# Optimization experiments

Measured on AMD Instinct MI355X. Metric: run time of the kernel, lower is better.

## Reference

```python
import jax, jax.numpy as jnp
import numpy as np
from jax import lax

HIDDEN = 1024; HEADS = 16; HEAD = 64; LAYERS = 4; MLP = 4096
PATCH = 16; TUBE = 2; CROP = 224; FRAMES = 16
GRID = CROP // PATCH          # 14
DEPTH = FRAMES // TUBE        # 8
N_TOK = DEPTH * GRID * GRID   # 1568
EPS = 1e-6
D_ROT = 2 * ((HEAD // 3) // 2)  # 20 per rotary axis (d, h, w); 4 dims left unrotated


def setup_inputs() -> dict:
    key = jax.random.key(0)
    ks = jax.random.split(key, 12)
    w = lambda k, shape: jax.random.normal(k, shape, jnp.float32) * 0.02
    L, H, M = LAYERS, HIDDEN, MLP
    return {
        "pixel_values_videos": jax.random.normal(ks[0], (2, FRAMES, 3, CROP, CROP), jnp.float32),
        "patch_w": w(ks[1], (H, 3, TUBE, PATCH, PATCH)),  # Conv3d OIDHW
        "patch_b": jnp.zeros((H,), jnp.float32),
        "ln1_g": jnp.ones((L, H), jnp.float32), "ln1_b": jnp.zeros((L, H), jnp.float32),
        "qw": w(ks[2], (L, H, H)), "qb": jnp.zeros((L, H), jnp.float32),
        "kw": w(ks[3], (L, H, H)), "kb": jnp.zeros((L, H), jnp.float32),
        "vw": w(ks[4], (L, H, H)), "vb": jnp.zeros((L, H), jnp.float32),
        "pw": w(ks[5], (L, H, H)), "pb": jnp.zeros((L, H), jnp.float32),
        "ln2_g": jnp.ones((L, H), jnp.float32), "ln2_b": jnp.zeros((L, H), jnp.float32),
        "fc1w": w(ks[6], (L, M, H)), "fc1b": jnp.zeros((L, M), jnp.float32),
        "fc2w": w(ks[7], (L, H, M)), "fc2b": jnp.zeros((L, H), jnp.float32),
        "lnf_g": jnp.ones((H,), jnp.float32), "lnf_b": jnp.zeros((H,), jnp.float32),
    }


def _layer_norm(x, g, b):
    mu = jnp.mean(x, axis=-1, keepdims=True)
    var = jnp.mean(jnp.square(x - mu), axis=-1, keepdims=True)
    return (x - mu) * lax.rsqrt(var + EPS) * g + b


def _position_ids():
    ids = jnp.arange(N_TOK)
    tpf = GRID * GRID
    d_pos = ids // tpf
    rem = ids - d_pos * tpf
    h_pos = rem // GRID
    w_pos = rem - h_pos * GRID
    return d_pos, h_pos, w_pos


def _rotate(x, pos):
    # x: (B, H, N, D); matches VJEPA2 rotate_queries_or_keys:
    # tiled (not interleaved) sin/cos * interleaved rotate-half.
    D = x.shape[-1]
    omega = 1.0 / (10000.0 ** (jnp.arange(D // 2, dtype=x.dtype) / (D / 2.0)))
    freq = pos.astype(x.dtype)[:, None] * omega              # (N, D/2)
    sin = jnp.concatenate([jnp.sin(freq)] * 2, axis=-1)      # (N, D) tiled (torch .repeat)
    cos = jnp.concatenate([jnp.cos(freq)] * 2, axis=-1)
    y = x.reshape(x.shape[:-1] + (D // 2, 2))
    y = jnp.stack([-y[..., 1], y[..., 0]], axis=-1).reshape(x.shape)
    return x * cos + y * sin


def _apply_rope(x, pos_ids):
    d_pos, h_pos, w_pos = pos_ids
    s0, s1, s2 = 0, D_ROT, 2 * D_ROT
    parts = [_rotate(x[..., s0:s1], d_pos), _rotate(x[..., s1:s2], h_pos),
             _rotate(x[..., s2:3 * D_ROT], w_pos)]
    if 3 * D_ROT < HEAD:
        parts.append(x[..., 3 * D_ROT:])
    return jnp.concatenate(parts, axis=-1)


def _forward(pixel_values_videos, patch_w, patch_b, ln1_g, ln1_b, qw, qb, kw, kb,
             vw, vb, pw, pb, ln2_g, ln2_b, fc1w, fc1b, fc2w, fc2b, lnf_g, lnf_b):
    B = pixel_values_videos.shape[0]
    x = jnp.transpose(pixel_values_videos, (0, 2, 1, 3, 4))  # (B, C, T, H, W)
    h = lax.conv_general_dilated(x, patch_w, window_strides=(TUBE, PATCH, PATCH),
                                 padding="VALID",
                                 dimension_numbers=("NCDHW", "OIDHW", "NCDHW"))
    h = h + patch_b[None, :, None, None, None]
    h = h.reshape(B, HIDDEN, -1).transpose(0, 2, 1)          # (B, N, HIDDEN)

    pos_ids = _position_ids()
    scale = HEAD ** -0.5

    for i in range(LAYERS):
        # attention block
        xn = _layer_norm(h, ln1_g[i], ln1_b[i])
        def heads(w_, b_):
            return (xn @ w_.T + b_).reshape(B, N_TOK, HEADS, HEAD).transpose(0, 2, 1, 3)
        q = _apply_rope(heads(qw[i], qb[i]), pos_ids)
        k = _apply_rope(heads(kw[i], kb[i]), pos_ids)
        v = heads(vw[i], vb[i])
        aw = jnp.einsum("bhnd,bhmd->bhnm", q, k) * scale
        aw = jax.nn.softmax(aw.astype(jnp.float32), axis=-1).astype(q.dtype)
        o = jnp.einsum("bhnm,bhmd->bhnd", aw, v)
        o = o.transpose(0, 2, 1, 3).reshape(B, N_TOK, HIDDEN)
        h = h + (o @ pw[i].T + pb[i])
        # MLP block
        xn = _layer_norm(h, ln2_g[i], ln2_b[i])
        m = jax.nn.gelu(xn @ fc1w[i].T + fc1b[i], approximate=False)
        h = h + (m @ fc2w[i].T + fc2b[i])

    return _layer_norm(h, lnf_g, lnf_b)


def reference(pixel_values_videos, patch_w, patch_b, ln1_g, ln1_b, qw, qb, kw, kb,
              vw, vb, pw, pb, ln2_g, ln2_b, fc1w, fc1b, fc2w, fc2b, lnf_g, lnf_b):
    return _forward(pixel_values_videos, patch_w, patch_b, ln1_g, ln1_b, qw, qb, kw, kb,
                    vw, vb, pw, pb, ln2_g, ln2_b, fc1w, fc1b, fc2w, fc2b, lnf_g, lnf_b)
```

## Files before the change

### kernel.cpp

```cpp
#include <hip/hip_runtime.h>
#include <math.h>

#define NTOK   1568
#define BATCH  2
#define HID    1024
#define MLPD   4096
#define NLAYER 4
#define ROWS   (BATCH*NTOK)
#define CONVK  1536

typedef __bf16 bf16x8 __attribute__((ext_vector_type(8)));
typedef float  f32x4  __attribute__((ext_vector_type(4)));

__device__ __forceinline__ unsigned short f2b(float f) {
  unsigned int u = __float_as_uint(f);
  unsigned int r = u + 0x7FFFu + ((u >> 16) & 1u);
  return (unsigned short)(r >> 16);
}
__device__ __forceinline__ float b2f(unsigned short s) {
  return __uint_as_float((unsigned int)s << 16);
}

__device__ __forceinline__ void async16(const unsigned short* g, unsigned short* l) {
  __builtin_amdgcn_global_load_lds(
      (__attribute__((address_space(1))) void*)(void*)g,
      (__attribute__((address_space(3))) void*)(void*)l, 16, 0, 0);
}

__global__ __launch_bounds__(256) void cast4_k(const float* __restrict__ s,
                                               unsigned short* __restrict__ d,
                                               long long n4) {
  long long i = (long long)blockIdx.x * 256 + threadIdx.x;
  long long stride = (long long)gridDim.x * 256;
  for (; i < n4; i += stride) {
    float4 v = ((const float4*)s)[i];
    *(ushort4*)(d + i * 4) = make_ushort4(f2b(v.x), f2b(v.y), f2b(v.z), f2b(v.w));
  }
}

__global__ __launch_bounds__(256) void castqkv_k(const float* __restrict__ q,
                                                 const float* __restrict__ k,
                                                 const float* __restrict__ v,
                                                 unsigned short* __restrict__ dst) {
  const float* src = blockIdx.y == 0 ? q : (blockIdx.y == 1 ? k : v);
  long long i4 = (long long)blockIdx.x * 256 + threadIdx.x;
  long long e = i4 * 4;
  int layer = (int)(e >> 20);
  long long de = e + ((long long)(2 * layer + blockIdx.y) << 20);
  float4 val = ((const float4*)src)[i4];
  *(ushort4*)(dst + de) = make_ushort4(f2b(val.x), f2b(val.y), f2b(val.z), f2b(val.w));
}

__global__ __launch_bounds__(256) void biascat_k(const float* __restrict__ qb,
                                                 const float* __restrict__ kb,
                                                 const float* __restrict__ vb,
                                                 float* __restrict__ dst) {
  int idx = blockIdx.x * 256 + threadIdx.x;
  int layer = idx / 3072, c = idx % 3072;
  float v = c < 1024 ? qb[layer * 1024 + c]
            : (c < 2048 ? kb[layer * 1024 + c - 1024] : vb[layer * 1024 + c - 2048]);
  dst[idx] = v;
}

__global__ __launch_bounds__(256) void im2col_k(const float* __restrict__ pv,
                                                unsigned short* __restrict__ A) {
  int idx = blockIdx.x * 256 + threadIdx.x;
  int row = idx / CONVK, col = idx % CONVK;
  int b = row / NTOK, t = row % NTOK;
  int d = t / 196, r = t % 196, hh = r / 14, ww = r % 14;
  int c = col >> 9, r2 = col & 511, td = r2 >> 8, ph = (r2 >> 4) & 15, pw = r2 & 15;
  int frame = 2 * d + td;
  const float* src = pv + ((((long long)b * 16 + frame) * 3 + c) * 224 + (hh * 16 + ph)) * 224
                        + (ww * 16 + pw);
  A[idx] = f2b(*src);
}

__global__ __launch_bounds__(256) void gemm_bt(const unsigned short* __restrict__ A,
                                               const unsigned short* __restrict__ B,
                                               unsigned short* __restrict__ outP,
                                               int M, int N, int K, int kChunk) {
  __shared__ unsigned short As[2][128 * 32];
  __shared__ unsigned short Bs[2][128 * 32];
  const int tid = threadIdx.x;
  const int lane = tid & 63;
  const int w = tid >> 6;
  const int wm = (w >> 1) * 64, wn = (w & 1) * 64;
  const int l15 = lane & 15, l4 = lane >> 4;
  const int bm = blockIdx.y, bn = blockIdx.x;
  const int wbase = tid & ~63;
  const int kbeg = blockIdx.z * kChunk;

  auto stage = [&](int buf, int k0) {
#pragma unroll
    for (int it = 0; it < 2; ++it) {
      int c = it * 256 + tid;
      int rowA = bm * 128 + (c >> 2);
      if (rowA >= M) rowA = M - 1;
      async16(A + (size_t)rowA * K + k0 + (c & 3) * 8, &As[buf][(it * 256 + wbase) * 8]);
      int rowB = bn * 128 + (c >> 2);
      async16(B + (size_t)rowB * K + k0 + (c & 3) * 8, &Bs[buf][(it * 256 + wbase) * 8]);
    }
  };

  f32x4 acc[4][4] = {};
  stage(0, kbeg);
  const int nIter = kChunk >> 5;

  for (int i = 0; i < nIter; ++i) {
    const int cur = i & 1;
    __syncthreads();
    if (i + 1 < nIter) stage(cur ^ 1, kbeg + (i + 1) * 32);

    bf16x8 af[4], bfr[4];
#pragma unroll
    for (int ii = 0; ii < 4; ++ii)
      af[ii] = *(const bf16x8*)&As[cur][(wm + ii * 16 + l15) * 32 + l4 * 8];
#pragma unroll
    for (int j = 0; j < 4; ++j)
      bfr[j] = *(const bf16x8*)&Bs[cur][(wn + j * 16 + l15) * 32 + l4 * 8];
#pragma unroll
    for (int ii = 0; ii < 4; ++ii)
#pragma unroll
      for (int j = 0; j < 4; ++j)
        acc[ii][j] = __builtin_amdgcn_mfma_f32_16x16x32_bf16(af[ii], bfr[j], acc[ii][j], 0, 0, 0);
  }

  unsigned short* pout = outP + (size_t)blockIdx.z * ((size_t)M * N);
#pragma unroll
  for (int ii = 0; ii < 4; ++ii) {
    int rowb = bm * 128 + wm + ii * 16 + l4 * 4;
#pragma unroll
    for (int r = 0; r < 4; ++r) {
      int rr = rowb + r;
      if (rr >= M) continue;
#pragma unroll
      for (int j = 0; j < 4; ++j) {
        int col = bn * 128 + wn + j * 16 + l15;
        pout[(size_t)rr * N + col] = f2b(acc[ii][j][r]);
      }
    }
  }
}

template <int NP, int RESID, int GELU, int OUTB>
__global__ __launch_bounds__(256) void reduceN_k(const unsigned short* __restrict__ p,
                                                 const float* __restrict__ bias,
                                                 const float* __restrict__ resid,
                                                 float* __restrict__ outF,
                                                 unsigned short* __restrict__ outB,
                                                 int MN, int N) {
  int i8 = blockIdx.x * 256 + threadIdx.x;
  int e = i8 * 8;
  float acc[8];
#pragma unroll
  for (int j = 0; j < 8; ++j) acc[j] = 0.0f;
#pragma unroll
  for (int pp = 0; pp < NP; ++pp) {
    const unsigned short* src = p + (size_t)pp * MN + e;
    ushort4 a0 = *(const ushort4*)src;
    ushort4 a1 = *(const ushort4*)(src + 4);
    acc[0] += b2f(a0.x); acc[1] += b2f(a0.y); acc[2] += b2f(a0.z); acc[3] += b2f(a0.w);
    acc[4] += b2f(a1.x); acc[5] += b2f(a1.y); acc[6] += b2f(a1.z); acc[7] += b2f(a1.w);
  }
  int col = e % N;
  float4 b0 = *(const float4*)(bias + col);
  float4 b1 = *(const float4*)(bias + col + 4);
  acc[0] += b0.x; acc[1] += b0.y; acc[2] += b0.z; acc[3] += b0.w;
  acc[4] += b1.x; acc[5] += b1.y; acc[6] += b1.z; acc[7] += b1.w;
  if (RESID) {
    float4 r0 = *(const float4*)(resid + e);
    float4 r1 = *(const float4*)(resid + e + 4);
    acc[0] += r0.x; acc[1] += r0.y; acc[2] += r0.z; acc[3] += r0.w;
    acc[4] += r1.x; acc[5] += r1.y; acc[6] += r1.z; acc[7] += r1.w;
  }
  if (GELU) {
#pragma unroll
    for (int j = 0; j < 8; ++j)
      acc[j] = 0.5f * acc[j] * (1.0f + erff(acc[j] * 0.70710678118654752f));
  }
  if (OUTB) {
    *(ushort4*)(outB + e) = make_ushort4(f2b(acc[0]), f2b(acc[1]), f2b(acc[2]), f2b(acc[3]));
    *(ushort4*)(outB + e + 4) = make_ushort4(f2b(acc[4]), f2b(acc[5]), f2b(acc[6]), f2b(acc[7]));
  } else {
    *(float4*)(outF + e) = make_float4(acc[0], acc[1], acc[2], acc[3]);
    *(float4*)(outF + e + 4) = make_float4(acc[4], acc[5], acc[6], acc[7]);
  }
}

template <int OUT_BF16>
__global__ __launch_bounds__(256) void ln_k(const float* __restrict__ x,
                                            const float* __restrict__ g,
                                            const float* __restrict__ b,
                                            unsigned short* __restrict__ oB,
                                            float* __restrict__ oF) {
  __shared__ float red[8];
  const int row = blockIdx.x, tid = threadIdx.x;
  const float4 v = ((const float4*)(x + (size_t)row * HID))[tid];
  float s = v.x + v.y + v.z + v.w;
  float q = v.x * v.x + v.y * v.y + v.z * v.z + v.w * v.w;
  for (int off = 32; off; off >>= 1) { s += __shfl_xor(s, off); q += __shfl_xor(q, off); }
  if ((tid & 63) == 0) { red[tid >> 6] = s; red[4 + (tid >> 6)] = q; }
  __syncthreads();
  float ts = red[0] + red[1] + red[2] + red[3];
  float tq = red[4] + red[5] + red[6] + red[7];
  float mu = ts * (1.0f / HID);
  float var = tq * (1.0f / HID) - mu * mu;
  float rs = rsqrtf(var + 1e-6f);
  int col = tid * 4;
  float o0 = (v.x - mu) * rs * g[col + 0] + b[col + 0];
  float o1 = (v.y - mu) * rs * g[col + 1] + b[col + 1];
  float o2 = (v.z - mu) * rs * g[col + 2] + b[col + 2];
  float o3 = (v.w - mu) * rs * g[col + 3] + b[col + 3];
  if (OUT_BF16) {
    *(ushort4*)(oB + (size_t)row * HID + col) = make_ushort4(f2b(o0), f2b(o1), f2b(o2), f2b(o3));
  } else {
    *(float4*)(oF + (size_t)row * HID + col) = make_float4(o0, o1, o2, o3);
  }
}

__global__ __launch_bounds__(256) void qkvprep_k(const unsigned short* __restrict__ qkvb,
                                                 unsigned short* __restrict__ Qh,
                                                 unsigned short* __restrict__ Kh,
                                                 unsigned short* __restrict__ VT) {
  __shared__ unsigned short Vs[64 * 72];
  const int tile = blockIdx.x, bh = blockIdx.y;
  const int b = bh >> 4, head = bh & 15;
  const int tid = threadIdx.x;
  const int tl = tid >> 2, dc = tid & 3;
  const int tg = tile * 64 + tl;
  const int trc = tg < NTOK ? tg : NTOK - 1;
  const bool valid = tg < NTOK;
  const size_t srow = ((size_t)(b * NTOK + trc)) * 3072 + head * 64 + dc * 16;

  {
    uint4 v0 = *(const uint4*)(qkvb + srow + 2048);
    uint4 v1 = *(const uint4*)(qkvb + srow + 2048 + 8);
    *(uint4*)&Vs[tl * 72 + dc * 16] = v0;
    *(uint4*)&Vs[tl * 72 + dc * 16 + 8] = v1;
  }

  const int t = trc;
  const int dpos = t / 196, rem = t - dpos * 196, hpos = rem / 14, wpos = rem - hpos * 14;
  const float LG = 0.9210340371976184f;
  union V16 { uint4 u[2]; unsigned short s[16]; };
  V16 qin, kin, qout, kout;
  qin.u[0] = *(const uint4*)(qkvb + srow);
  qin.u[1] = *(const uint4*)(qkvb + srow + 8);
  kin.u[0] = *(const uint4*)(qkvb + srow + 1024);
  kin.u[1] = *(const uint4*)(qkvb + srow + 1024 + 8);
#pragma unroll
  for (int p = 0; p < 8; ++p) {
    int d0 = dc * 16 + 2 * p;
    float qx0 = b2f(qin.s[2 * p]), qx1 = b2f(qin.s[2 * p + 1]);
    float kx0 = b2f(kin.s[2 * p]), kx1 = b2f(kin.s[2 * p + 1]);
    float qo0, qo1, ko0, ko1;
    if (d0 >= 60) { qo0 = qx0; qo1 = qx1; ko0 = kx0; ko1 = kx1; }
    else {
      int region = d0 / 20;
      int j0 = d0 - region * 20;
      int pos = region == 0 ? dpos : (region == 1 ? hpos : wpos);
      float fp = (float)pos;
      int i0 = j0 % 10, i1 = (j0 + 1) % 10;
      float f0 = expf(-LG * (float)i0) * fp;
      float f1 = expf(-LG * (float)i1) * fp;
      float c0 = cosf(f0), s0 = sinf(f0), c1 = cosf(f1), s1 = sinf(f1);
      qo0 = qx0 * c0 - qx1 * s0; qo1 = qx1 * c1 + qx0 * s1;
      ko0 = kx0 * c0 - kx1 * s0; ko1 = kx1 * c1 + kx0 * s1;
    }
    qout.s[2 * p]     = f2b(qo0 * 0.125f);
    qout.s[2 * p + 1] = f2b(qo1 * 0.125f);
    kout.s[2 * p]     = f2b(ko0);
    kout.s[2 * p + 1] = f2b(ko1);
  }
  if (valid) {
    size_t drow = ((size_t)bh * NTOK + tg) * 64 + dc * 16;
    *(uint4*)(Qh + drow)     = qout.u[0];
    *(uint4*)(Qh + drow + 8) = qout.u[1];
    *(uint4*)(Kh + drow)     = kout.u[0];
    *(uint4*)(Kh + drow + 8) = kout.u[1];
  }
  __syncthreads();
  {
    int d = tid >> 2, tc = tid & 3;
    if (tile * 64 + tc * 16 < NTOK) {
      V16 o;
#pragma unroll
      for (int jj = 0; jj < 16; ++jj) o.s[jj] = Vs[(tc * 16 + jj) * 72 + d];
      unsigned short* dst = VT + ((size_t)bh * 64 + d) * NTOK + tile * 64 + tc * 16;
      *(uint4*)dst = o.u[0];
      *(uint4*)(dst + 8) = o.u[1];
    }
  }
}

__global__ __launch_bounds__(256, 3) void flash4_k(const unsigned short* __restrict__ Qh,
                                                   const unsigned short* __restrict__ Kh,
                                                   const unsigned short* __restrict__ VT,
                                                   unsigned short* __restrict__ O) {
  __shared__ unsigned short Ks[2][64 * 64];
  __shared__ unsigned short Vs[2][64 * 64];
  __shared__ unsigned short Os[4][16 * 72];
  const int bh = blockIdx.x, qt = blockIdx.y;
  const int b = bh >> 4, head = bh & 15;
  const int tid = threadIdx.x, lane = tid & 63, w = tid >> 6;
  const int l15 = lane & 15, l4 = lane >> 4;
  const size_t hb = (size_t)bh * NTOK * 64;
  const unsigned short* kgp = Kh + hb;
  const unsigned short* vbp = VT + (size_t)bh * 64 * NTOK;

  const int srow0 = w * 8 + (lane >> 3);
  const int scg0  = (lane & 7) ^ (srow0 & 7);
  const int srow1 = srow0 + 32;
  const int scg1  = (lane & 7) ^ (srow1 & 7);

  const int qrow = qt * 64 + w * 16 + l15;
  const int qrc = qrow < NTOK ? qrow : NTOK - 1;
  bf16x8 q0 = *(const bf16x8*)(Qh + hb + (size_t)qrc * 64 + l4 * 8);
  bf16x8 q1 = *(const bf16x8*)(Qh + hb + (size_t)qrc * 64 + 32 + l4 * 8);

  f32x4 oacc[4] = {};
  float m = -1e30f, l = 0.0f;

  {
    async16(kgp + (size_t)srow0 * 64 + scg0 * 8, &Ks[0][(size_t)w * 512]);
    async16(kgp + (size_t)srow1 * 64 + scg1 * 8, &Ks[0][(size_t)(w + 4) * 512]);
    async16(vbp + (size_t)srow0 * NTOK + scg0 * 8, &Vs[0][(size_t)w * 512]);
    async16(vbp + (size_t)srow1 * NTOK + scg1 * 8, &Vs[0][(size_t)(w + 4) * 512]);
  }

  const int h7 = l15 & 7;
  const int p1 = (l4 ^ h7) * 8;
  const int p2 = ((l4 + 4) ^ h7) * 8;

  for (int kt = 0; kt < 25; ++kt) {
    const int cur = kt & 1, nxt = cur ^ 1;
    const int kb = kt * 64;
    __syncthreads();

    if (kt < 24) {
      const int kn = kb + 64;
      async16(kgp + (size_t)(kn + srow0) * 64 + scg0 * 8, &Ks[nxt][(size_t)w * 512]);
      async16(kgp + (size_t)(kn + srow1) * 64 + scg1 * 8, &Ks[nxt][(size_t)(w + 4) * 512]);
      async16(vbp + (size_t)srow0 * NTOK + kn + scg0 * 8, &Vs[nxt][(size_t)w * 512]);
      async16(vbp + (size_t)srow1 * NTOK + kn + scg1 * 8, &Vs[nxt][(size_t)(w + 4) * 512]);
    }

    bf16x8 kc0[4], kc1[4];
#pragma unroll
    for (int nt = 0; nt < 4; ++nt) {
      const unsigned short* kr = &Ks[cur][(nt * 16 + l15) * 64];
      kc0[nt] = *(const bf16x8*)(kr + p1);
      kc1[nt] = *(const bf16x8*)(kr + p2);
    }
    f32x4 s[4] = {};
#pragma unroll
    for (int nt = 0; nt < 4; ++nt) {
      s[nt] = __builtin_amdgcn_mfma_f32_16x16x32_bf16(kc0[nt], q0, s[nt], 0, 0, 0);
      s[nt] = __builtin_amdgcn_mfma_f32_16x16x32_bf16(kc1[nt], q1, s[nt], 0, 0, 0);
    }
    bf16x8 vf0[4], vf1[4];
#pragma unroll
    for (int dt = 0; dt < 4; ++dt) {
      const unsigned short* vr = &Vs[cur][(dt * 16 + l15) * 64];
      vf0[dt] = *(const bf16x8*)(vr + p1);
      vf1[dt] = *(const bf16x8*)(vr + p2);
    }

    if (kb + 64 > NTOK) {
#pragma unroll
      for (int nt = 0; nt < 4; ++nt)
#pragma unroll
        for (int r = 0; r < 4; ++r)
          if (kb + nt * 16 + l4 * 4 + r >= NTOK) s[nt][r] = -1e30f;
    }
    float rmax = s[0][0];
#pragma unroll
    for (int nt = 0; nt < 4; ++nt)
#pragma unroll
      for (int r = 0; r < 4; ++r) rmax = fmaxf(rmax, s[nt][r]);
    rmax = fmaxf(rmax, __shfl_xor(rmax, 16));
    rmax = fmaxf(rmax, __shfl_xor(rmax, 32));
    float mn = fmaxf(m, rmax);
    float alpha = __expf(m - mn);
    m = mn;
    float rsum = 0.0f;
#pragma unroll
    for (int nt = 0; nt < 4; ++nt)
#pragma unroll
      for (int r = 0; r < 4; ++r) {
        float p = __expf(s[nt][r] - mn);
        s[nt][r] = p;
        rsum += p;
      }
    rsum += __shfl_xor(rsum, 16);
    rsum += __shfl_xor(rsum, 32);
    l = l * alpha + rsum;
#pragma unroll
    for (int dt = 0; dt < 4; ++dt)
#pragma unroll
      for (int r = 0; r < 4; ++r) oacc[dt][r] *= alpha;

    unsigned pk01[4], pk23[4];
#pragma unroll
    for (int nt = 0; nt < 4; ++nt) {
      pk01[nt] = (unsigned)f2b(s[nt][0]) | ((unsigned)f2b(s[nt][1]) << 16);
      pk23[nt] = (unsigned)f2b(s[nt][2]) | ((unsigned)f2b(s[nt][3]) << 16);
    }
    const int srcA = ((l4 & 1) << 5) | l15;
    const int srcB = srcA + 16;
    const bool hi = (l4 >> 1) != 0;
    union PB { unsigned u[4]; bf16x8 v; } pf[2];
#pragma unroll
    for (int kc = 0; kc < 2; ++kc) {
      unsigned t0, t1;
      t0 = __shfl(pk01[2 * kc], srcA); t1 = __shfl(pk01[2 * kc + 1], srcA);
      pf[kc].u[0] = hi ? t1 : t0;
      t0 = __shfl(pk23[2 * kc], srcA); t1 = __shfl(pk23[2 * kc + 1], srcA);
      pf[kc].u[1] = hi ? t1 : t0;
      t0 = __shfl(pk01[2 * kc], srcB); t1 = __shfl(pk01[2 * kc + 1], srcB);
      pf[kc].u[2] = hi ? t1 : t0;
      t0 = __shfl(pk23[2 * kc], srcB); t1 = __shfl(pk23[2 * kc + 1], srcB);
      pf[kc].u[3] = hi ? t1 : t0;
    }
#pragma unroll
    for (int dt = 0; dt < 4; ++dt) {
      oacc[dt] = __builtin_amdgcn_mfma_f32_16x16x32_bf16(vf0[dt], pf[0].v, oacc[dt], 0, 0, 0);
      oacc[dt] = __builtin_amdgcn_mfma_f32_16x16x32_bf16(vf1[dt], pf[1].v, oacc[dt], 0, 0, 0);
    }
  }

  float inv = 1.0f / l;
#pragma unroll
  for (int dt = 0; dt < 4; ++dt)
#pragma unroll
    for (int r = 0; r < 4; ++r)
      Os[w][l15 * 72 + dt * 16 + l4 * 4 + r] = f2b(oacc[dt][r] * inv);
  if (qrow < NTOK) {
    uint4 a  = *(const uint4*)&Os[w][l15 * 72 + l4 * 16];
    uint4 bq = *(const uint4*)&Os[w][l15 * 72 + l4 * 16 + 8];
    unsigned short* op = O + ((size_t)(b * NTOK + qrow)) * HID + head * 64;
    *(uint4*)(op + l4 * 16) = a;
    *(uint4*)(op + l4 * 16 + 8) = bq;
  }
}

extern "C" void kernel_launch(void* const* d_in, const int* in_sizes, int n_in,
                              void* d_out, int out_size, void* d_ws, size_t ws_size,
                              hipStream_t stream) {
  (void)in_sizes; (void)n_in; (void)out_size; (void)ws_size;
  const float* pv      = (const float*)d_in[0];
  const float* patch_w = (const float*)d_in[1];
  const float* patch_b = (const float*)d_in[2];
  const float* ln1_g   = (const float*)d_in[3];
  const float* ln1_b   = (const float*)d_in[4];
  const float* qw = (const float*)d_in[5];
  const float* qb = (const float*)d_in[6];
  const float* kw = (const float*)d_in[7];
  const float* kb = (const float*)d_in[8];
  const float* vw = (const float*)d_in[9];
  const float* vb = (const float*)d_in[10];
  const float* pw = (const float*)d_in[11];
  const float* pb = (const float*)d_in[12];
  const float* ln2_g = (const float*)d_in[13];
  const float* ln2_b = (const float*)d_in[14];
  const float* fc1w = (const float*)d_in[15];
  const float* fc1b = (const float*)d_in[16];
  const float* fc2w = (const float*)d_in[17];
  const float* fc2b = (const float*)d_in[18];
  const float* lnf_g = (const float*)d_in[19];
  const float* lnf_b = (const float*)d_in[20];

  char* wsp = (char*)d_ws;
  auto alloc = [&](size_t bytes) {
    char* p = wsp;
    wsp += (bytes + 255) & ~(size_t)255;
    return p;
  };
  unsigned short* wPatch = (unsigned short*)alloc((size_t)1024 * 1536 * 2);
  unsigned short* wQKV   = (unsigned short*)alloc((size_t)NLAYER * 3072 * 1024 * 2);
  unsigned short* wP     = (unsigned short*)alloc((size_t)NLAYER * HID * HID * 2);
  unsigned short* wF1    = (unsigned short*)alloc((size_t)NLAYER * MLPD * HID * 2);
  unsigned short* wF2    = (unsigned short*)alloc((size_t)NLAYER * HID * MLPD * 2);
  float*          qkvbias = (float*)alloc((size_t)NLAYER * 3072 * 4);
  unsigned short* Aim  = (unsigned short*)alloc((size_t)ROWS * CONVK * 2);
  float*          h    = (float*)alloc((size_t)ROWS * HID * 4);
  unsigned short* xnb  = (unsigned short*)alloc((size_t)ROWS * HID * 2);
  unsigned short* qkvo = (unsigned short*)alloc((size_t)ROWS * 3072 * 2);
  unsigned short* Qh   = (unsigned short*)alloc((size_t)ROWS * HID * 2 + 8192);
  unsigned short* Kh   = (unsigned short*)alloc((size_t)ROWS * HID * 2 + 8192);
  unsigned short* VT   = (unsigned short*)alloc((size_t)ROWS * HID * 2 + 8192);
  unsigned short* ob   = (unsigned short*)alloc((size_t)ROWS * HID * 2);
  unsigned short* mb   = (unsigned short*)alloc((size_t)ROWS * MLPD * 2);
  unsigned short* part = Qh;

  const int MN = ROWS * HID;

  auto cast = [&](const float* s, unsigned short* d, long long n) {
    long long n4 = n / 4;
    int grid = (int)((n4 + 255) / 256);
    if (grid > 16384) grid = 16384;
    cast4_k<<<grid, 256, 0, stream>>>(s, d, n4);
  };
  cast(patch_w, wPatch, (long long)1024 * 1536);
  castqkv_k<<<dim3(4096, 3), 256, 0, stream>>>(qw, kw, vw, wQKV);
  cast(pw, wP, (long long)NLAYER * HID * HID);
  cast(fc1w, wF1, (long long)NLAYER * MLPD * HID);
  cast(fc2w, wF2, (long long)NLAYER * HID * MLPD);
  biascat_k<<<48, 256, 0, stream>>>(qb, kb, vb, qkvbias);

  im2col_k<<<(ROWS * CONVK) / 256, 256, 0, stream>>>(pv, Aim);
  gemm_bt<<<dim3(8, 25, 3), 256, 0, stream>>>(Aim, wPatch, part, ROWS, HID, CONVK, 512);
  reduceN_k<3, 0, 0, 0><<<MN / 2048, 256, 0, stream>>>(
      part, patch_b, nullptr, h, nullptr, MN, HID);

  for (int i = 0; i < NLAYER; ++i) {
    ln_k<1><<<ROWS, 256, 0, stream>>>(h, ln1_g + i * HID, ln1_b + i * HID, xnb, nullptr);
    gemm_bt<<<dim3(24, 25, 2), 256, 0, stream>>>(
        xnb, wQKV + (size_t)i * 3072 * 1024, part, ROWS, 3072, HID, 512);
    reduceN_k<2, 0, 0, 1><<<(ROWS * 3072) / 2048, 256, 0, stream>>>(
        part, qkvbias + i * 3072, nullptr, nullptr, qkvo, ROWS * 3072, 3072);
    qkvprep_k<<<dim3(25, 32), 256, 0, stream>>>(qkvo, Qh, Kh, VT);
    flash4_k<<<dim3(32, 25), 256, 0, stream>>>(Qh, Kh, VT, ob);
    gemm_bt<<<dim3(8, 25, 4), 256, 0, stream>>>(
        ob, wP + (size_t)i * HID * HID, part, ROWS, HID, HID, 256);
    reduceN_k<4, 1, 0, 0><<<MN / 2048, 256, 0, stream>>>(
        part, pb + i * HID, h, h, nullptr, MN, HID);
    ln_k<1><<<ROWS, 256, 0, stream>>>(h, ln2_g + i * HID, ln2_b + i * HID, xnb, nullptr);
    gemm_bt<<<dim3(32, 25, 2), 256, 0, stream>>>(
        xnb, wF1 + (size_t)i * MLPD * HID, part, ROWS, MLPD, HID, 512);
    reduceN_k<2, 0, 1, 1><<<(ROWS * MLPD) / 2048, 256, 0, stream>>>(
        part, fc1b + i * MLPD, nullptr, nullptr, mb, ROWS * MLPD, MLPD);
    gemm_bt<<<dim3(8, 25, 4), 256, 0, stream>>>(
        mb, wF2 + (size_t)i * HID * MLPD, part, ROWS, HID, MLPD, 1024);
    reduceN_k<4, 1, 0, 0><<<MN / 2048, 256, 0, stream>>>(
        part, fc2b + i * HID, h, h, nullptr, MN, HID);
  }
  ln_k<0><<<ROWS, 256, 0, stream>>>(h, lnf_g, lnf_b, nullptr, (float*)d_out);
}
```

Before: 1.505 ms.

## Fuse split-K reduction with LayerNorm and split attention KV across two blocks

Replaces the separate split-K reduce plus LayerNorm kernels with one redln_k that sums partials, adds bias and residual, writes h and emits the normalized bf16 activations, including the final LayerNorm. This removes a full read/write pass over the hidden state per residual point. Attention is split into two KV halves (flash5_k, grid z=2, higher occupancy bound) with a combine kernel that merges the partial outputs using the saved max and sum, adding parallelism at the cost of an extra bf16 partial round-trip. Partial buffers are re-aliased across existing allocations with explicit strides, which depends on careful buffer lifetime reasoning.

```diff
diff --git a/kernel.cpp b/kernel.cpp
--- a/kernel.cpp
+++ b/kernel.cpp
@@ -77,8 +77,9 @@
 
 __global__ __launch_bounds__(256) void gemm_bt(const unsigned short* __restrict__ A,
                                                const unsigned short* __restrict__ B,
-                                               unsigned short* __restrict__ outP,
-                                               int M, int N, int K, int kChunk) {
+                                               unsigned short* outP,
+                                               int M, int N, int K, int kChunk,
+                                               size_t zStride) {
   __shared__ unsigned short As[2][128 * 32];
   __shared__ unsigned short Bs[2][128 * 32];
   const int tid = threadIdx.x;
@@ -125,7 +126,7 @@
         acc[ii][j] = __builtin_amdgcn_mfma_f32_16x16x32_bf16(af[ii], bfr[j], acc[ii][j], 0, 0, 0);
   }
 
-  unsigned short* pout = outP + (size_t)blockIdx.z * ((size_t)M * N);
+  unsigned short* pout = outP + (size_t)blockIdx.z * zStride;
 #pragma unroll
   for (int ii = 0; ii < 4; ++ii) {
     int rowb = bm * 128 + wm + ii * 16 + l4 * 4;
@@ -142,13 +143,11 @@
   }
 }
 
-template <int NP, int RESID, int GELU, int OUTB>
-__global__ __launch_bounds__(256) void reduceN_k(const unsigned short* __restrict__ p,
+template <int NP, int GELU>
+__global__ __launch_bounds__(256) void reduceN_k(const unsigned short* p,
                                                  const float* __restrict__ bias,
-                                                 const float* __restrict__ resid,
-                                                 float* __restrict__ outF,
-                                                 unsigned short* __restrict__ outB,
-                                                 int MN, int N) {
+                                                 unsigned short* outB,
+                                                 int MN, int N, size_t pStride) {
   int i8 = blockIdx.x * 256 + threadIdx.x;
   int e = i8 * 8;
   float acc[8];
@@ -156,7 +155,7 @@
   for (int j = 0; j < 8; ++j) acc[j] = 0.0f;
 #pragma unroll
   for (int pp = 0; pp < NP; ++pp) {
-    const unsigned short* src = p + (size_t)pp * MN + e;
+    const unsigned short* src = p + (size_t)pp * pStride + e;
     ushort4 a0 = *(const ushort4*)src;
     ushort4 a1 = *(const ushort4*)(src + 4);
     acc[0] += b2f(a0.x); acc[1] += b2f(a0.y); acc[2] += b2f(a0.z); acc[3] += b2f(a0.w);
@@ -167,38 +166,45 @@
   float4 b1 = *(const float4*)(bias + col + 4);
   acc[0] += b0.x; acc[1] += b0.y; acc[2] += b0.z; acc[3] += b0.w;
   acc[4] += b1.x; acc[5] += b1.y; acc[6] += b1.z; acc[7] += b1.w;
-  if (RESID) {
-    float4 r0 = *(const float4*)(resid + e);
-    float4 r1 = *(const float4*)(resid + e + 4);
-    acc[0] += r0.x; acc[1] += r0.y; acc[2] += r0.z; acc[3] += r0.w;
-    acc[4] += r1.x; acc[5] += r1.y; acc[6] += r1.z; acc[7] += r1.w;
-  }
   if (GELU) {
 #pragma unroll
     for (int j = 0; j < 8; ++j)
       acc[j] = 0.5f * acc[j] * (1.0f + erff(acc[j] * 0.70710678118654752f));
   }
-  if (OUTB) {
-    *(ushort4*)(outB + e) = make_ushort4(f2b(acc[0]), f2b(acc[1]), f2b(acc[2]), f2b(acc[3]));
-    *(ushort4*)(outB + e + 4) = make_ushort4(f2b(acc[4]), f2b(acc[5]), f2b(acc[6]), f2b(acc[7]));
-  } else {
-    *(float4*)(outF + e) = make_float4(acc[0], acc[1], acc[2], acc[3]);
-    *(float4*)(outF + e + 4) = make_float4(acc[4], acc[5], acc[6], acc[7]);
-  }
-}
-
-template <int OUT_BF16>
-__global__ __launch_bounds__(256) void ln_k(const float* __restrict__ x,
-                                            const float* __restrict__ g,
-                                            const float* __restrict__ b,
-                                            unsigned short* __restrict__ oB,
-                                            float* __restrict__ oF) {
+  *(ushort4*)(outB + e) = make_ushort4(f2b(acc[0]), f2b(acc[1]), f2b(acc[2]), f2b(acc[3]));
+  *(ushort4*)(outB + e + 4) = make_ushort4(f2b(acc[4]), f2b(acc[5]), f2b(acc[6]), f2b(acc[7]));
+}
+
+template <int NP, int RESID, int FINAL>
+__global__ __launch_bounds__(256) void redln_k(const unsigned short* __restrict__ p,
+                                               const float* __restrict__ bias,
+                                               const float* resid,
+                                               const float* __restrict__ g,
+                                               const float* __restrict__ b,
+                                               float* hOut,
+                                               unsigned short* __restrict__ xnOut,
+                                               float* __restrict__ fOut,
+                                               size_t pStride) {
   __shared__ float red[8];
   const int row = blockIdx.x, tid = threadIdx.x;
-  const float4 v = ((const float4*)(x + (size_t)row * HID))[tid];
-  float s = v.x + v.y + v.z + v.w;
-  float q = v.x * v.x + v.y * v.y + v.z * v.z + v.w * v.w;
-  for (int off = 32; off; off >>= 1) { s += __shfl_xor(s, off); q += __shfl_xor(q, off); }
+  const int col = tid * 4;
+  const size_t off = (size_t)row * HID + col;
+  float v0 = 0, v1 = 0, v2 = 0, v3 = 0;
+#pragma unroll
+  for (int pp = 0; pp < NP; ++pp) {
+    ushort4 a = *(const ushort4*)(p + (size_t)pp * pStride + off);
+    v0 += b2f(a.x); v1 += b2f(a.y); v2 += b2f(a.z); v3 += b2f(a.w);
+  }
+  float4 bs = *(const float4*)(bias + col);
+  v0 += bs.x; v1 += bs.y; v2 += bs.z; v3 += bs.w;
+  if (RESID) {
+    float4 r = *(const float4*)(resid + off);
+    v0 += r.x; v1 += r.y; v2 += r.z; v3 += r.w;
+  }
+  if (!FINAL) *(float4*)(hOut + off) = make_float4(v0, v1, v2, v3);
+  float s = v0 + v1 + v2 + v3;
+  float q = v0 * v0 + v1 * v1 + v2 * v2 + v3 * v3;
+  for (int o2 = 32; o2; o2 >>= 1) { s += __shfl_xor(s, o2); q += __shfl_xor(q, o2); }
   if ((tid & 63) == 0) { red[tid >> 6] = s; red[4 + (tid >> 6)] = q; }
   __syncthreads();
   float ts = red[0] + red[1] + red[2] + red[3];
@@ -206,15 +212,14 @@
   float mu = ts * (1.0f / HID);
   float var = tq * (1.0f / HID) - mu * mu;
   float rs = rsqrtf(var + 1e-6f);
-  int col = tid * 4;
-  float o0 = (v.x - mu) * rs * g[col + 0] + b[col + 0];
-  float o1 = (v.y - mu) * rs * g[col + 1] + b[col + 1];
-  float o2 = (v.z - mu) * rs * g[col + 2] + b[col + 2];
-  float o3 = (v.w - mu) * rs * g[col + 3] + b[col + 3];
-  if (OUT_BF16) {
-    *(ushort4*)(oB + (size_t)row * HID + col) = make_ushort4(f2b(o0), f2b(o1), f2b(o2), f2b(o3));
+  float o0 = (v0 - mu) * rs * g[col + 0] + b[col + 0];
+  float o1 = (v1 - mu) * rs * g[col + 1] + b[col + 1];
+  float o2 = (v2 - mu) * rs * g[col + 2] + b[col + 2];
+  float o3 = (v3 - mu) * rs * g[col + 3] + b[col + 3];
+  if (FINAL) {
+    *(float4*)(fOut + off) = make_float4(o0, o1, o2, o3);
   } else {
-    *(float4*)(oF + (size_t)row * HID + col) = make_float4(o0, o1, o2, o3);
+    *(ushort4*)(xnOut + off) = make_ushort4(f2b(o0), f2b(o1), f2b(o2), f2b(o3));
   }
 }
 
@@ -293,15 +298,15 @@
   }
 }
 
-__global__ __launch_bounds__(256, 3) void flash4_k(const unsigned short* __restrict__ Qh,
+__global__ __launch_bounds__(256, 4) void flash5_k(const unsigned short* __restrict__ Qh,
                                                    const unsigned short* __restrict__ Kh,
                                                    const unsigned short* __restrict__ VT,
-                                                   unsigned short* __restrict__ O) {
+                                                   unsigned short* __restrict__ Opart,
+                                                   float2* __restrict__ ml) {
   __shared__ unsigned short Ks[2][64 * 64];
   __shared__ unsigned short Vs[2][64 * 64];
-  __shared__ unsigned short Os[4][16 * 72];
-  const int bh = blockIdx.x, qt = blockIdx.y;
-  const int b = bh >> 4, head = bh & 15;
+  const int bh = blockIdx.x, qt = blockIdx.y, kv = blockIdx.z;
+  const int kt0 = kv ? 13 : 0, kt1 = kv ? 25 : 13;
   const int tid = threadIdx.x, lane = tid & 63, w = tid >> 6;
   const int l15 = lane & 15, l4 = lane >> 4;
   const size_t hb = (size_t)bh * NTOK * 64;
@@ -322,22 +327,23 @@
   float m = -1e30f, l = 0.0f;
 
   {
-    async16(kgp + (size_t)srow0 * 64 + scg0 * 8, &Ks[0][(size_t)w * 512]);
-    async16(kgp + (size_t)srow1 * 64 + scg1 * 8, &Ks[0][(size_t)(w + 4) * 512]);
-    async16(vbp + (size_t)srow0 * NTOK + scg0 * 8, &Vs[0][(size_t)w * 512]);
-    async16(vbp + (size_t)srow1 * NTOK + scg1 * 8, &Vs[0][(size_t)(w + 4) * 512]);
+    const int kc0 = kt0 * 64;
+    async16(kgp + (size_t)(kc0 + srow0) * 64 + scg0 * 8, &Ks[0][(size_t)w * 512]);
+    async16(kgp + (size_t)(kc0 + srow1) * 64 + scg1 * 8, &Ks[0][(size_t)(w + 4) * 512]);
+    async16(vbp + (size_t)srow0 * NTOK + kc0 + scg0 * 8, &Vs[0][(size_t)w * 512]);
+    async16(vbp + (size_t)srow1 * NTOK + kc0 + scg1 * 8, &Vs[0][(size_t)(w + 4) * 512]);
   }
 
   const int h7 = l15 & 7;
   const int p1 = (l4 ^ h7) * 8;
   const int p2 = ((l4 + 4) ^ h7) * 8;
 
-  for (int kt = 0; kt < 25; ++kt) {
-    const int cur = kt & 1, nxt = cur ^ 1;
+  for (int kt = kt0; kt < kt1; ++kt) {
+    const int cur = (kt - kt0) & 1, nxt = cur ^ 1;
     const int kb = kt * 64;
     __syncthreads();
 
-    if (kt < 24) {
+    if (kt + 1 < kt1) {
       const int kn = kb + 64;
       async16(kgp + (size_t)(kn + srow0) * 64 + scg0 * 8, &Ks[nxt][(size_t)w * 512]);
       async16(kgp + (size_t)(kn + srow1) * 64 + scg1 * 8, &Ks[nxt][(size_t)(w + 4) * 512]);
@@ -429,19 +435,48 @@
     }
   }
 
-  float inv = 1.0f / l;
+  __syncthreads();
+  unsigned short* Os = &Ks[0][0];
 #pragma unroll
   for (int dt = 0; dt < 4; ++dt)
 #pragma unroll
     for (int r = 0; r < 4; ++r)
-      Os[w][l15 * 72 + dt * 16 + l4 * 4 + r] = f2b(oacc[dt][r] * inv);
+      Os[w * 1152 + l15 * 72 + dt * 16 + l4 * 4 + r] = f2b(oacc[dt][r]);
   if (qrow < NTOK) {
-    uint4 a  = *(const uint4*)&Os[w][l15 * 72 + l4 * 16];
-    uint4 bq = *(const uint4*)&Os[w][l15 * 72 + l4 * 16 + 8];
-    unsigned short* op = O + ((size_t)(b * NTOK + qrow)) * HID + head * 64;
+    uint4 a  = *(const uint4*)&Os[w * 1152 + l15 * 72 + l4 * 16];
+    uint4 bq = *(const uint4*)&Os[w * 1152 + l15 * 72 + l4 * 16 + 8];
+    unsigned short* op = Opart + ((size_t)(kv * 32 + bh) * NTOK + qrow) * 64;
     *(uint4*)(op + l4 * 16) = a;
     *(uint4*)(op + l4 * 16 + 8) = bq;
-  }
+    if (l4 == 0) ml[(size_t)(kv * 32 + bh) * NTOK + qrow] = make_float2(m, l);
+  }
+}
+
+__global__ __launch_bounds__(256) void fcomb_k(const unsigned short* __restrict__ Op,
+                                               const float2* __restrict__ ml,
+                                               unsigned short* __restrict__ O) {
+  const int bh = blockIdx.x, qt = blockIdx.y;
+  const int tid = threadIdx.x;
+  const int qr = qt * 64 + (tid >> 2);
+  const int dc = (tid & 3) * 16;
+  if (qr >= NTOK) return;
+  const int b = bh >> 4, head = bh & 15;
+  float2 a0 = ml[(size_t)bh * NTOK + qr];
+  float2 a1 = ml[(size_t)(32 + bh) * NTOK + qr];
+  float M = fmaxf(a0.x, a1.x);
+  float w0 = __expf(a0.x - M), w1 = __expf(a1.x - M);
+  float inv = 1.0f / (a0.y * w0 + a1.y * w1);
+  w0 *= inv; w1 *= inv;
+  union V16 { uint4 u[2]; unsigned short s[16]; } p0, p1, o;
+  const unsigned short* q0 = Op + ((size_t)bh * NTOK + qr) * 64 + dc;
+  const unsigned short* q1 = Op + ((size_t)(32 + bh) * NTOK + qr) * 64 + dc;
+  p0.u[0] = *(const uint4*)q0;       p0.u[1] = *(const uint4*)(q0 + 8);
+  p1.u[0] = *(const uint4*)q1;       p1.u[1] = *(const uint4*)(q1 + 8);
+#pragma unroll
+  for (int j = 0; j < 16; ++j) o.s[j] = f2b(b2f(p0.s[j]) * w0 + b2f(p1.s[j]) * w1);
+  unsigned short* dst = O + ((size_t)(b * NTOK + qr)) * HID + head * 64 + dc;
+  *(uint4*)dst = o.u[0];
+  *(uint4*)(dst + 8) = o.u[1];
 }
 
 extern "C" void kernel_launch(void* const* d_in, const int* in_sizes, int n_in,
@@ -491,9 +526,13 @@
   unsigned short* VT   = (unsigned short*)alloc((size_t)ROWS * HID * 2 + 8192);
   unsigned short* ob   = (unsigned short*)alloc((size_t)ROWS * HID * 2);
   unsigned short* mb   = (unsigned short*)alloc((size_t)ROWS * MLPD * 2);
-  unsigned short* part = Qh;
-
-  const int MN = ROWS * HID;
+
+  unsigned short* part  = Qh;
+  unsigned short* partM = mb;
+  unsigned short* Opart = mb;
+  float2*         mlbuf = (float2*)(mb + (size_t)2 * 32 * NTOK * 64);
+  const size_t MNs = (size_t)ROWS * HID;
+  const size_t strideF1 = (size_t)(mb - part);
 
   auto cast = [&](const float* s, unsigned short* d, long long n) {
     long long n4 = n / 4;
@@ -509,31 +548,36 @@
   biascat_k<<<48, 256, 0, stream>>>(qb, kb, vb, qkvbias);
 
   im2col_k<<<(ROWS * CONVK) / 256, 256, 0, stream>>>(pv, Aim);
-  gemm_bt<<<dim3(8, 25, 3), 256, 0, stream>>>(Aim, wPatch, part, ROWS, HID, CONVK, 512);
-  reduceN_k<3, 0, 0, 0><<<MN / 2048, 256, 0, stream>>>(
-      part, patch_b, nullptr, h, nullptr, MN, HID);
+  gemm_bt<<<dim3(8, 25, 3), 256, 0, stream>>>(Aim, wPatch, part, ROWS, HID, CONVK, 512, MNs);
+  redln_k<3, 0, 0><<<ROWS, 256, 0, stream>>>(
+      part, patch_b, nullptr, ln1_g, ln1_b, h, xnb, nullptr, MNs);
 
   for (int i = 0; i < NLAYER; ++i) {
-    ln_k<1><<<ROWS, 256, 0, stream>>>(h, ln1_g + i * HID, ln1_b + i * HID, xnb, nullptr);
     gemm_bt<<<dim3(24, 25, 2), 256, 0, stream>>>(
-        xnb, wQKV + (size_t)i * 3072 * 1024, part, ROWS, 3072, HID, 512);
-    reduceN_k<2, 0, 0, 1><<<(ROWS * 3072) / 2048, 256, 0, stream>>>(
-        part, qkvbias + i * 3072, nullptr, nullptr, qkvo, ROWS * 3072, 3072);
+        xnb, wQKV + (size_t)i * 3072 * 1024, part, ROWS, 3072, HID, 512,
+        (size_t)ROWS * 3072);
+    reduceN_k<2, 0><<<(ROWS * 3072) / 2048, 256, 0, stream>>>(
+        part, qkvbias + i * 3072, qkvo, ROWS * 3072, 3072, (size_t)ROWS * 3072);
     qkvprep_k<<<dim3(25, 32), 256, 0, stream>>>(qkvo, Qh, Kh, VT);
-    flash4_k<<<dim3(32, 25), 256, 0, stream>>>(Qh, Kh, VT, ob);
+    flash5_k<<<dim3(32, 25, 2), 256, 0, stream>>>(Qh, Kh, VT, Opart, mlbuf);
+    fcomb_k<<<dim3(32, 25), 256, 0, stream>>>(Opart, mlbuf, ob);
     gemm_bt<<<dim3(8, 25, 4), 256, 0, stream>>>(
-        ob, wP + (size_t)i * HID * HID, part, ROWS, HID, HID, 256);
-    reduceN_k<4, 1, 0, 0><<<MN / 2048, 256, 0, stream>>>(
-        part, pb + i * HID, h, h, nullptr, MN, HID);
-    ln_k<1><<<ROWS, 256, 0, stream>>>(h, ln2_g + i * HID, ln2_b + i * HID, xnb, nullptr);
+        ob, wP + (size_t)i * HID * HID, partM, ROWS, HID, HID, 256, MNs);
+    redln_k<4, 1, 0><<<ROWS, 256, 0, stream>>>(
+        partM, pb + i * HID, h, ln2_g + i * HID, ln2_b + i * HID, h, xnb, nullptr, MNs);
     gemm_bt<<<dim3(32, 25, 2), 256, 0, stream>>>(
-        xnb, wF1 + (size_t)i * MLPD * HID, part, ROWS, MLPD, HID, 512);
-    reduceN_k<2, 0, 1, 1><<<(ROWS * MLPD) / 2048, 256, 0, stream>>>(
-        part, fc1b + i * MLPD, nullptr, nullptr, mb, ROWS * MLPD, MLPD);
+        xnb, wF1 + (size_t)i * MLPD * HID, part, ROWS, MLPD, HID, 512, strideF1);
+    reduceN_k<2, 1><<<(ROWS * MLPD) / 2048, 256, 0, stream>>>(
+        part, fc1b + i * MLPD, mb, ROWS * MLPD, MLPD, strideF1);
     gemm_bt<<<dim3(8, 25, 4), 256, 0, stream>>>(
-        mb, wF2 + (size_t)i * HID * MLPD, part, ROWS, HID, MLPD, 1024);
-    reduceN_k<4, 1, 0, 0><<<MN / 2048, 256, 0, stream>>>(
-        part, fc2b + i * HID, h, h, nullptr, MN, HID);
-  }
-  ln_k<0><<<ROWS, 256, 0, stream>>>(h, lnf_g, lnf_b, nullptr, (float*)d_out);
-}
+        mb, wF2 + (size_t)i * HID * MLPD, part, ROWS, HID, MLPD, 1024, MNs);
+    if (i < NLAYER - 1) {
+      redln_k<4, 1, 0><<<ROWS, 256, 0, stream>>>(
+          part, fc2b + i * HID, h, ln1_g + (i + 1) * HID, ln1_b + (i + 1) * HID,
+          h, xnb, nullptr, MNs);
+    } else {
+      redln_k<4, 1, 1><<<ROWS, 256, 0, stream>>>(
+          part, fc2b + i * HID, h, lnf_g, lnf_b, nullptr, nullptr, (float*)d_out, MNs);
+    }
+  }
+}
```

After: 1.406 ms. 6.6% less time.
